# Kernel optimization log

Hardware: AMD Instinct MI355X
Metric: run time of the kernel (lower is better)

The kernel has to match this reference:

```python
import jax, jax.numpy as jnp
import numpy as np

B, C, H, W = 8, 256, 48, 48
G = 32  # num_groups
EPS = 1e-5


def setup_inputs() -> dict:
    key = jax.random.key(0)
    ks = jax.random.split(key, 9)
    s = 0.02
    return {
        "input": jax.random.normal(ks[0], (B, C, H, W), dtype=jnp.float32),
        "Wq": jax.random.normal(ks[1], (C, C), dtype=jnp.float32) * s,
        "bq": jnp.zeros((C,), dtype=jnp.float32),
        "Wk": jax.random.normal(ks[2], (C, C), dtype=jnp.float32) * s,
        "bk": jnp.zeros((C,), dtype=jnp.float32),
        "Wv": jax.random.normal(ks[3], (C, C), dtype=jnp.float32) * s,
        "bv": jnp.zeros((C,), dtype=jnp.float32),
        "gn_w": jnp.ones((C,), dtype=jnp.float32),
        "gn_b": jnp.zeros((C,), dtype=jnp.float32),
    }


def _group_norm(x, w, b):
    # x: [B, C, H, W] -> normalize per (group) over (C//G, H, W)
    n, c, h, wd = x.shape
    xg = x.reshape(n, G, c // G, h, wd)
    mean = jnp.mean(xg, axis=(2, 3, 4), keepdims=True)
    var = jnp.var(xg, axis=(2, 3, 4), keepdims=True)
    xg = (xg - mean) * jax.lax.rsqrt(var + EPS)
    x = xg.reshape(n, c, h, wd)
    return x * w[None, :, None, None] + b[None, :, None, None]


def _conv1x1(x, wgt, bias):
    # 1x1 conv == per-pixel channel GEMM. wgt: [C_out, C_in]
    return jnp.einsum('bchw,oc->bohw', x, wgt) + bias[None, :, None, None]


def reference(input, Wq, bq, Wk, bk, Wv, bv, gn_w, gn_b):
    x = _group_norm(input, gn_w, gn_b)
    q = _conv1x1(x, Wq, bq)
    k = _conv1x1(x, Wk, bk)
    v = _conv1x1(x, Wv, bv)
    d = q.shape[1]
    # energy[b,h,w,h',w'] = sum_c q[b,c,h,w] * k[b,c,h',w'] / sqrt(d)
    energy = jnp.einsum('bchw,bcef->bhwef', q, k) / jnp.sqrt(jnp.float32(d))
    n, h, w2 = energy.shape[0], energy.shape[1], energy.shape[2]
    energy = jax.nn.softmax(energy.reshape(n, h, w2, h * w2), axis=-1)
    energy = energy.reshape(n, h, w2, h, w2)
    # out[b,c,h,w] = sum_{h',w'} energy[b,h,w,h',w'] * v[b,c,h',w']
    out = jnp.einsum('bhwef,bcef->bchw', energy, v)
    return out
```

## Files before the change

### kernel.cpp

```cpp
#include <hip/hip_runtime.h>
#include <math.h>

#define NB 8
#define NC 256
#define NHW 2304
#define NG 32
#define CPG 8
#define GN_EPS 1e-5f
#define ATT_SCALE 0.0625f
#define XSTR 258

typedef __bf16 bf16x8 __attribute__((ext_vector_type(8)));
typedef __bf16 bf16x4 __attribute__((ext_vector_type(4)));
typedef float f32x4 __attribute__((ext_vector_type(4)));

#define MFMA(a, b, c) __builtin_amdgcn_mfma_f32_16x16x32_bf16(a, b, c, 0, 0, 0)

__device__ __forceinline__ void async_lds16(const void* g, void* l) {
  __builtin_amdgcn_global_load_lds(
      (const __attribute__((address_space(1))) void*)g,
      (__attribute__((address_space(3))) void*)l, 16, 0, 0);
}

__global__ __launch_bounds__(256) void k_prep(
    const float* __restrict__ x, const float* __restrict__ gn_w,
    const float* __restrict__ gn_b, float* __restrict__ scale,
    float* __restrict__ shift,
    const float* __restrict__ Wq, const float* __restrict__ Wk,
    const float* __restrict__ Wv, __bf16* __restrict__ Wqb,
    __bf16* __restrict__ Wkb, __bf16* __restrict__ Wvb) {
  __shared__ float red[8];
  int blk = blockIdx.x;
  if (blk >= 256) {
    int idx = blk - 256;
    int which = idx >> 6;
    const float* src = which == 0 ? Wq : (which == 1 ? Wk : Wv);
    __bf16* dst = which == 0 ? Wqb : (which == 1 ? Wkb : Wvb);
    int i = (idx & 63) * 256 + threadIdx.x;
    float4 v = ((const float4*)src)[i];
    bf16x4 o;
    o[0] = (__bf16)v.x; o[1] = (__bf16)v.y;
    o[2] = (__bf16)v.z; o[3] = (__bf16)v.w;
    ((bf16x4*)dst)[i] = o;
    return;
  }
  const float4* base = (const float4*)(x + (size_t)blk * CPG * NHW);
  const int n4 = CPG * NHW / 4;
  float s = 0.f, ss = 0.f;
  for (int i = threadIdx.x; i < n4; i += 256) {
    float4 v = base[i];
    s  += v.x + v.y + v.z + v.w;
    ss += v.x * v.x + v.y * v.y + v.z * v.z + v.w * v.w;
  }
  for (int off = 32; off > 0; off >>= 1) {
    s  += __shfl_down(s, off);
    ss += __shfl_down(ss, off);
  }
  int wv = threadIdx.x >> 6, ln = threadIdx.x & 63;
  if (ln == 0) { red[wv] = s; red[4 + wv] = ss; }
  __syncthreads();
  if (threadIdx.x < CPG) {
    float S  = red[0] + red[1] + red[2] + red[3];
    float SS = red[4] + red[5] + red[6] + red[7];
    const float inv_n = 1.f / (float)(CPG * NHW);
    float mean = S * inv_n;
    float var  = SS * inv_n - mean * mean;
    float rstd = rsqrtf(var + GN_EPS);
    int b = blk / NG, g = blk % NG;
    int c = g * CPG + threadIdx.x;
    float sc = gn_w[c] * rstd;
    scale[b * NC + c] = sc;
    shift[b * NC + c] = gn_b[c] - mean * sc;
  }
}

__global__ __launch_bounds__(256) void k_xnT(
    const float* __restrict__ x, const float* __restrict__ scale,
    const float* __restrict__ shift, __bf16* __restrict__ xnT) {
  __shared__ __bf16 t[64 * XSTR];
  int p0 = blockIdx.x * 64;
  int b = blockIdx.y;
  int w = threadIdx.x >> 6, lane = threadIdx.x & 63;
  const float* xb = x + (size_t)b * NC * NHW;
  const float* scb = scale + b * NC;
  const float* shb = shift + b * NC;
#pragma unroll 8
  for (int i = 0; i < 64; ++i) {
    int c = i * 4 + w;
    float v = xb[(size_t)c * NHW + p0 + lane] * scb[c] + shb[c];
    t[lane * XSTR + c] = (__bf16)v;
  }
  __syncthreads();
#pragma unroll
  for (int i = 0; i < 8; ++i) {
    int row = i * 8 + w * 2 + (lane >> 5);
    int c8 = (lane & 31) * 8;
    bf16x8 v8 = *(const bf16x8*)&t[row * XSTR + c8];
    *(bf16x8*)&xnT[((size_t)b * NHW + p0 + row) * NC + c8] = v8;
  }
}

__global__ __launch_bounds__(256) void k_qkv(
    const __bf16* __restrict__ xnT,
    const __bf16* __restrict__ Wqb, const __bf16* __restrict__ Wkb,
    const __bf16* __restrict__ Wvb,
    const float* __restrict__ bq, const float* __restrict__ bk,
    const float* __restrict__ bv,
    __bf16* __restrict__ qT, __bf16* __restrict__ kT,
    __bf16* __restrict__ vbuf) {
  __shared__ __bf16 tile[9216];
  int blk = blockIdx.x;
  int b = blk & 7;
  int r = blk >> 3;
  int oq = r & 3;
  int pg = r >> 2;
  int p0 = pg * 128, o0 = oq * 64;
  int tid = threadIdx.x;
  int w = tid >> 6, lane = tid & 63;
  int col = lane & 15, quad = lane >> 4;

  const __bf16* xrow =
      xnT + ((size_t)b * NHW + p0 + w * 32 + col) * NC + quad * 8;
  bf16x8 xf[2][8];
#pragma unroll
  for (int mt = 0; mt < 2; ++mt)
#pragma unroll
    for (int ks = 0; ks < 8; ++ks)
      xf[mt][ks] = *(const bf16x8*)(xrow + (size_t)mt * 16 * NC + ks * 32);

#pragma unroll
  for (int t = 0; t < 3; ++t) {
    const __bf16* W = t == 0 ? Wqb : (t == 1 ? Wkb : Wvb);
    const float* bias = t == 0 ? bq : (t == 1 ? bk : bv);
    f32x4 acc[2][4];
#pragma unroll
    for (int mt = 0; mt < 2; ++mt)
#pragma unroll
      for (int nt = 0; nt < 4; ++nt) acc[mt][nt] = (f32x4){0.f, 0.f, 0.f, 0.f};
#pragma unroll
    for (int nt = 0; nt < 4; ++nt) {
      const __bf16* wrow = W + ((size_t)(o0 + nt * 16 + col)) * NC + quad * 8;
#pragma unroll
      for (int ks = 0; ks < 8; ++ks) {
        bf16x8 wf = *(const bf16x8*)(wrow + ks * 32);
        acc[0][nt] = MFMA(xf[0][ks], wf, acc[0][nt]);
        acc[1][nt] = MFMA(xf[1][ks], wf, acc[1][nt]);
      }
    }
    if (t > 0) __syncthreads();
    if (t < 2) {
#pragma unroll
      for (int mt = 0; mt < 2; ++mt)
#pragma unroll
        for (int nt = 0; nt < 4; ++nt) {
          float bc = bias[o0 + nt * 16 + col];
#pragma unroll
          for (int reg = 0; reg < 4; ++reg) {
            int row = w * 32 + mt * 16 + quad * 4 + reg;
            tile[row * 72 + nt * 16 + col] = (__bf16)(acc[mt][nt][reg] + bc);
          }
        }
      __syncthreads();
      __bf16* dst = t == 0 ? qT : kT;
#pragma unroll
      for (int pass = 0; pass < 4; ++pass) {
        int unit = pass * 256 + tid;
        int row = unit >> 3, ch = unit & 7;
        bf16x8 v8 = *(const bf16x8*)&tile[row * 72 + ch * 8];
        *(bf16x8*)&dst[((size_t)b * NHW + p0 + row) * NC + o0 + ch * 8] = v8;
      }
    } else {
#pragma unroll
      for (int mt = 0; mt < 2; ++mt)
#pragma unroll
        for (int nt = 0; nt < 4; ++nt) {
          float bc = bias[o0 + nt * 16 + col];
#pragma unroll
          for (int reg = 0; reg < 4; ++reg) {
            int p = w * 32 + mt * 16 + quad * 4 + reg;
            tile[(nt * 16 + col) * 136 + p] = (__bf16)(acc[mt][nt][reg] + bc);
          }
        }
      __syncthreads();
#pragma unroll
      for (int pass = 0; pass < 4; ++pass) {
        int unit = pass * 256 + tid;
        int row = unit >> 4, ch = unit & 15;
        bf16x8 v8 = *(const bf16x8*)&tile[row * 136 + ch * 8];
        *(bf16x8*)&vbuf[((size_t)b * NC + o0 + row) * NHW + p0 + ch * 8] = v8;
      }
    }
  }
}

__global__ __launch_bounds__(256, 2) void k_fused(
    const __bf16* __restrict__ qT, const __bf16* __restrict__ kT,
    const __bf16* __restrict__ vbuf, float* __restrict__ opart,
    float* __restrict__ lpart) {
  __shared__ __bf16 sk[64 * 256];
  __shared__ __bf16 sv[256 * 64];
  __shared__ __bf16 sp[64 * 64];
  __shared__ float slsum[2][64];

  int blk = blockIdx.x;
  int b = blk & 7;
  int r = blk >> 3;
  int kh = r & 1;
  int qg = r >> 1;
  int q0 = qg * 64;
  int tid = threadIdx.x;
  int w = tid >> 6, lane = tid & 63;
  int wm = w >> 1, wn = w & 1;
  int col = lane & 15, quad = lane >> 4;
  int c7 = col & 7;

  auto stage_kv = [&](int it2) {
    int k0 = (kh * 18 + it2) * 64;
    {
      int sub = lane >> 5, p5 = lane & 31;
#pragma unroll
      for (int j = 0; j < 8; ++j) {
        int r0 = w * 16 + j * 2;
        int rloc = r0 + sub;
        int g = p5 ^ (rloc & 7);
        async_lds16(kT + ((size_t)b * NHW + k0 + rloc) * NC + g * 8,
                    (void*)&sk[r0 * 256]);
      }
    }
    {
      int sub = lane >> 3, p3 = lane & 7;
#pragma unroll
      for (int j = 0; j < 8; ++j) {
        int r0 = w * 64 + j * 8;
        int rloc = r0 + sub;
        int g = p3 ^ (rloc & 7);
        async_lds16(vbuf + ((size_t)b * NC + rloc) * NHW + k0 + g * 8,
                    (void*)&sv[r0 * 64]);
      }
    }
  };

  const __bf16* qrow =
      qT + ((size_t)b * NHW + q0 + wn * 32 + col) * NC + quad * 8;
  bf16x8 qf[2][8];
#pragma unroll
  for (int nt = 0; nt < 2; ++nt)
#pragma unroll
    for (int ks = 0; ks < 8; ++ks)
      qf[nt][ks] = *(const bf16x8*)(qrow + (size_t)nt * 16 * NC + ks * 32);

  stage_kv(0);

  f32x4 acc[4][4];
#pragma unroll
  for (int mt = 0; mt < 4; ++mt)
#pragma unroll
    for (int nt = 0; nt < 4; ++nt) acc[mt][nt] = (f32x4){0.f, 0.f, 0.f, 0.f};
  float lsum_r[2] = {0.f, 0.f};

  for (int it = 0; it < 18; ++it) {
    __syncthreads();

    f32x4 sacc[2][2];
#pragma unroll
    for (int mt = 0; mt < 2; ++mt)
#pragma unroll
      for (int nt = 0; nt < 2; ++nt) sacc[mt][nt] = (f32x4){0.f, 0.f, 0.f, 0.f};
#pragma unroll
    for (int ks = 0; ks < 8; ++ks) {
#pragma unroll
      for (int mt = 0; mt < 2; ++mt) {
        int krow = wm * 32 + mt * 16 + col;
        bf16x8 kf = *(const bf16x8*)
            &sk[krow * 256 + (((ks * 4 + quad) ^ c7) << 3)];
        sacc[mt][0] = MFMA(kf, qf[0][ks], sacc[mt][0]);
        sacc[mt][1] = MFMA(kf, qf[1][ks], sacc[mt][1]);
      }
    }

#pragma unroll
    for (int nt = 0; nt < 2; ++nt) {
      float ps = 0.f;
      int q = wn * 32 + nt * 16 + col;
#pragma unroll
      for (int mt = 0; mt < 2; ++mt) {
        bf16x4 pk;
#pragma unroll
        for (int reg = 0; reg < 4; ++reg) {
          float e = __expf(sacc[mt][nt][reg] * ATT_SCALE);
          ps += e;
          pk[reg] = (__bf16)e;
        }
        int chunk = (wm * 4 + mt * 2 + (quad >> 1)) ^ c7;
        *(bf16x4*)&sp[q * 64 + chunk * 8 + (quad & 1) * 4] = pk;
      }
      ps += __shfl_xor(ps, 16);
      ps += __shfl_xor(ps, 32);
      lsum_r[nt] += ps;
    }

    __syncthreads();

    bf16x8 pf[4][2], vf[4][2];
#pragma unroll
    for (int nt = 0; nt < 4; ++nt) {
      int q = nt * 16 + col;
#pragma unroll
      for (int ks = 0; ks < 2; ++ks)
        pf[nt][ks] = *(const bf16x8*)
            &sp[q * 64 + (((ks * 4 + quad) ^ c7) << 3)];
    }
#pragma unroll
    for (int mt = 0; mt < 4; ++mt) {
      int crow = w * 64 + mt * 16 + col;
#pragma unroll
      for (int ks = 0; ks < 2; ++ks)
        vf[mt][ks] = *(const bf16x8*)
            &sv[crow * 64 + (((ks * 4 + quad) ^ c7) << 3)];
    }
    if (it < 17) {
      asm volatile("s_waitcnt lgkmcnt(0)" ::: "memory");
      __builtin_amdgcn_sched_barrier(0);
      stage_kv(it + 1);
    }

#pragma unroll
    for (int mt = 0; mt < 4; ++mt)
#pragma unroll
      for (int nt = 0; nt < 4; ++nt) {
        acc[mt][nt] = MFMA(vf[mt][0], pf[nt][0], acc[mt][nt]);
        acc[mt][nt] = MFMA(vf[mt][1], pf[nt][1], acc[mt][nt]);
      }
  }

  if (quad == 0) {
#pragma unroll
    for (int nt = 0; nt < 2; ++nt)
      slsum[wm][wn * 32 + nt * 16 + col] = lsum_r[nt];
  }
  __syncthreads();

  float* opb = opart + (size_t)kh * NB * NC * NHW + (size_t)b * NC * NHW;
  float* lpb = lpart + (size_t)kh * NB * NHW + (size_t)b * NHW + q0;
#pragma unroll
  for (int nt = 0; nt < 4; ++nt) {
    int q = nt * 16 + col;
    float lsumv = slsum[0][q] + slsum[1][q];
    if (w == 0 && quad == 0) lpb[q] = lsumv;
#pragma unroll
    for (int mt = 0; mt < 4; ++mt) {
#pragma unroll
      for (int reg = 0; reg < 4; ++reg) {
        int c = w * 64 + mt * 16 + quad * 4 + reg;
        opb[(size_t)c * NHW + q0 + q] = acc[mt][nt][reg];
      }
    }
  }
}

__global__ __launch_bounds__(256) void k_comb(
    const float* __restrict__ opart, const float* __restrict__ lpart,
    float* __restrict__ out) {
  int i = blockIdx.x * 256 + threadIdx.x;
  const float4* o0 = (const float4*)opart;
  const float4* o1 = (const float4*)(opart + (size_t)NB * NC * NHW);
  float4 a = o0[i], c = o1[i];
  int flat = i * 4;
  int q = flat % NHW;
  int b = flat / (NC * NHW);
  const float4* l0 = (const float4*)lpart;
  const float4* l1 = (const float4*)(lpart + NB * NHW);
  int li = (b * NHW + q) >> 2;
  float4 s = l0[li], t = l1[li];
  float4 rr;
  rr.x = (a.x + c.x) / (s.x + t.x);
  rr.y = (a.y + c.y) / (s.y + t.y);
  rr.z = (a.z + c.z) / (s.z + t.z);
  rr.w = (a.w + c.w) / (s.w + t.w);
  ((float4*)out)[i] = rr;
}

extern "C" void kernel_launch(void* const* d_in, const int* in_sizes, int n_in,
                              void* d_out, int out_size, void* d_ws,
                              size_t ws_size, hipStream_t stream) {
  const float* x   = (const float*)d_in[0];
  const float* Wq  = (const float*)d_in[1];
  const float* bq  = (const float*)d_in[2];
  const float* Wk  = (const float*)d_in[3];
  const float* bk  = (const float*)d_in[4];
  const float* Wv  = (const float*)d_in[5];
  const float* bv  = (const float*)d_in[6];
  const float* gnw = (const float*)d_in[7];
  const float* gnb = (const float*)d_in[8];
  float* out = (float*)d_out;

  const size_t per = (size_t)NB * NC * NHW;
  char* wsb = (char*)d_ws;
  __bf16* qT   = (__bf16*)wsb;
  __bf16* kT   = (__bf16*)(wsb + per * 2);
  __bf16* vbuf = (__bf16*)(wsb + per * 4);
  __bf16* xnT  = (__bf16*)(wsb + per * 6);
  float* opart = (float*)(wsb + per * 6);
  float* lpart = (float*)(wsb + per * 14);
  char* tail   = wsb + per * 14 + (size_t)2 * NB * NHW * 4;
  __bf16* Wqb  = (__bf16*)tail;
  __bf16* Wkb  = Wqb + NC * NC;
  __bf16* Wvb  = Wkb + NC * NC;
  float* scale = (float*)(Wvb + NC * NC);
  float* shift = scale + NB * NC;

  hipLaunchKernelGGL(k_prep, dim3(448), dim3(256), 0, stream,
                     x, gnw, gnb, scale, shift, Wq, Wk, Wv, Wqb, Wkb, Wvb);
  hipLaunchKernelGGL(k_xnT, dim3(NHW / 64, NB), dim3(256), 0, stream,
                     x, scale, shift, xnT);
  hipLaunchKernelGGL(k_qkv, dim3(576), dim3(256), 0, stream,
                     xnT, Wqb, Wkb, Wvb, bq, bk, bv, qT, kT, vbuf);
  hipLaunchKernelGGL(k_fused, dim3(576), dim3(256), 0, stream,
                     qT, kT, vbuf, opart, lpart);
  hipLaunchKernelGGL(k_comb, dim3(4608), dim3(256), 0, stream,
                     opart, lpart, out);
}
```

Baseline: 255.4 us.

## Double-buffer K/V tiles in LDS with two-ahead async prefetch

Splits the K and V shared-memory tiles into two buffers and prefetches tile it+2 while computing on tile it. Uses vmcnt-based waits and raw barriers instead of __syncthreads, so global-to-LDS loads overlap a full iteration of compute. This doubles K/V LDS use, which likely limits residency to one block per CU and adds an extra barrier per iteration.

After: 258.6 us. About the same (+1.3%).

```diff
diff --git a/kernel.cpp b/kernel.cpp
--- a/kernel.cpp
+++ b/kernel.cpp
@@ -197,8 +197,8 @@
     const __bf16* __restrict__ qT, const __bf16* __restrict__ kT,
     const __bf16* __restrict__ vbuf, float* __restrict__ opart,
     float* __restrict__ lpart) {
-  __shared__ __bf16 sk[64 * 256];
-  __shared__ __bf16 sv[256 * 64];
+  __shared__ __bf16 sk[2][64 * 256];
+  __shared__ __bf16 sv[2][256 * 64];
   __shared__ __bf16 sp[64 * 64];
   __shared__ float slsum[2][64];
 
@@ -214,7 +214,7 @@
   int col = lane & 15, quad = lane >> 4;
   int c7 = col & 7;
 
-  auto stage_kv = [&](int it2) {
+  auto stage_kv = [&](int it2, int bsel) {
     int k0 = (kh * 18 + it2) * 64;
     {
       int sub = lane >> 5, p5 = lane & 31;
@@ -224,7 +224,7 @@
         int rloc = r0 + sub;
         int g = p5 ^ (rloc & 7);
         async_lds16(kT + ((size_t)b * NHW + k0 + rloc) * NC + g * 8,
-                    (void*)&sk[r0 * 256]);
+                    (void*)&sk[bsel][r0 * 256]);
       }
     }
     {
@@ -235,7 +235,7 @@
         int rloc = r0 + sub;
         int g = p3 ^ (rloc & 7);
         async_lds16(vbuf + ((size_t)b * NC + rloc) * NHW + k0 + g * 8,
-                    (void*)&sv[r0 * 64]);
+                    (void*)&sv[bsel][r0 * 64]);
       }
     }
   };
@@ -249,7 +249,8 @@
     for (int ks = 0; ks < 8; ++ks)
       qf[nt][ks] = *(const bf16x8*)(qrow + (size_t)nt * 16 * NC + ks * 32);
 
-  stage_kv(0);
+  stage_kv(0, 0);
+  stage_kv(1, 1);
 
   f32x4 acc[4][4];
 #pragma unroll
@@ -259,7 +260,15 @@
   float lsum_r[2] = {0.f, 0.f};
 
   for (int it = 0; it < 18; ++it) {
-    __syncthreads();
+    int cur = it & 1;
+    if (it < 17)
+      asm volatile("s_waitcnt vmcnt(16)" ::: "memory");
+    else
+      asm volatile("s_waitcnt vmcnt(0)" ::: "memory");
+    __builtin_amdgcn_s_barrier();
+
+    const __bf16* skc = sk[cur];
+    const __bf16* svc = sv[cur];
 
     f32x4 sacc[2][2];
 #pragma unroll
@@ -272,7 +281,7 @@
       for (int mt = 0; mt < 2; ++mt) {
         int krow = wm * 32 + mt * 16 + col;
         bf16x8 kf = *(const bf16x8*)
-            &sk[krow * 256 + (((ks * 4 + quad) ^ c7) << 3)];
+            &skc[krow * 256 + (((ks * 4 + quad) ^ c7) << 3)];
         sacc[mt][0] = MFMA(kf, qf[0][ks], sacc[mt][0]);
         sacc[mt][1] = MFMA(kf, qf[1][ks], sacc[mt][1]);
       }
@@ -299,7 +308,8 @@
       lsum_r[nt] += ps;
     }
 
-    __syncthreads();
+    asm volatile("s_waitcnt lgkmcnt(0)" ::: "memory");
+    __builtin_amdgcn_s_barrier();
 
     bf16x8 pf[4][2], vf[4][2];
 #pragma unroll
@@ -316,13 +326,14 @@
 #pragma unroll
       for (int ks = 0; ks < 2; ++ks)
         vf[mt][ks] = *(const bf16x8*)
-            &sv[crow * 64 + (((ks * 4 + quad) ^ c7) << 3)];
-    }
-    if (it < 17) {
-      asm volatile("s_waitcnt lgkmcnt(0)" ::: "memory");
-      __builtin_amdgcn_sched_barrier(0);
-      stage_kv(it + 1);
-    }
+            &svc[crow * 64 + (((ks * 4 + quad) ^ c7) << 3)];
+    }
+    asm volatile("s_waitcnt lgkmcnt(0)" ::: "memory");
+    __builtin_amdgcn_sched_barrier(0);
+    __builtin_amdgcn_s_barrier();
+
+    if (it < 16) stage_kv(it + 2, cur);
+    __builtin_amdgcn_sched_barrier(0);
 
 #pragma unroll
     for (int mt = 0; mt < 4; ++mt)
```
